# Kernel optimization log

Hardware: AMD Instinct MI355X
Metric: run time of the kernel (lower is better)

Reference implementation:

```python
import jax, jax.numpy as jnp
import numpy as np

B, S, E, H = 2, 2048, 1024, 16
DH = E // H
SCALE = DH ** -0.5

def setup_inputs() -> dict:
    key = jax.random.key(0)
    ks = jax.random.split(key, 5)
    w_std = (2.0 / (E + E)) ** 0.5  # xavier-ish scale
    return {
        'x': jax.random.normal(ks[0], (B, S, E), jnp.float32),
        'Wq': jax.random.normal(ks[1], (E, E), jnp.float32) * w_std,
        'bq': jnp.zeros((E,), jnp.float32),
        'Wk': jax.random.normal(ks[2], (E, E), jnp.float32) * w_std,
        'bk': jnp.zeros((E,), jnp.float32),
        'Wv': jax.random.normal(ks[3], (E, E), jnp.float32) * w_std,
        'bv': jnp.zeros((E,), jnp.float32),
        'Wo': jax.random.normal(ks[4], (E, E), jnp.float32) * w_std,
        'bo': jnp.zeros((E,), jnp.float32),
    }

def reference(x, Wq, bq, Wk, bk, Wv, bv, Wo, bo):
    # self-attention: query = key = value = x; torch Linear: y = x @ W.T + b
    q = (x @ Wq.T + bq) * SCALE            # [B,S,E]
    k = x @ Wk.T + bk
    v = x @ Wv.T + bv
    # split heads -> [B,S,H,DH]
    q = q.reshape(B, S, H, DH)
    k = k.reshape(B, S, H, DH)
    v = v.reshape(B, S, H, DH)
    # explicit attention matrix [B,H,S,S] (faithful to unfused bmm path)
    scores = jnp.einsum('bqhd,bkhd->bhqk', q, k)
    probs = jax.nn.softmax(scores, axis=-1)
    attn = jnp.einsum('bhqk,bkhd->bqhd', probs, v).reshape(B, S, E)
    return attn @ Wo.T + bo                # [B,S,E]
```

## Files before the change

### kernel.cpp

```cpp
#include <hip/hip_runtime.h>
#include <stdint.h>

#define BB 2
#define SS 2048
#define EE 1024
#define HH 16
#define DHD 64
#define MM (BB*SS)
#define QSCALE (0.125f * 1.4426950408889634f)

typedef __bf16 bf16;
typedef __bf16 bf16x8 __attribute__((ext_vector_type(8)));
typedef __bf16 bf16x4 __attribute__((ext_vector_type(4)));
typedef float  f32x4  __attribute__((ext_vector_type(4)));
typedef unsigned short ushort8 __attribute__((ext_vector_type(8)));

#define MFMA16(a,b,c) __builtin_amdgcn_mfma_f32_16x16x32_bf16(a,b,c,0,0,0)

__device__ __forceinline__ void gload_lds16(const void* g, void* l) {
  __builtin_amdgcn_global_load_lds(
      (const __attribute__((address_space(1))) unsigned int*)g,
      (__attribute__((address_space(3))) unsigned int*)l, 16, 0, 0);
}

__device__ __forceinline__ unsigned short f2bf(float f) {
  union { float f; unsigned u; } v; v.f = f;
  return (unsigned short)((v.u + 0x7FFFu + ((v.u >> 16) & 1u)) >> 16);
}

__global__ void convert_kernel(const float* __restrict__ x,
                               const float* __restrict__ wq, const float* __restrict__ wk,
                               const float* __restrict__ wv, const float* __restrict__ wo,
                               unsigned short* __restrict__ xbf,
                               unsigned short* __restrict__ wqb, unsigned short* __restrict__ wkb,
                               unsigned short* __restrict__ wvb, unsigned short* __restrict__ wob) {
  long t = (long)blockIdx.x * blockDim.x + threadIdx.x;
  long base = t * 8;
  const float* src; unsigned short* dst; long off;
  if (base < 4194304L) { src = x; dst = xbf; off = base; }
  else {
    long r = base - 4194304L; int j = (int)(r >> 20); off = r & 1048575L;
    src = (j==0)?wq:(j==1)?wk:(j==2)?wv:wo;
    dst = (j==0)?wqb:(j==1)?wkb:(j==2)?wvb:wob;
  }
  const float4* s4 = (const float4*)(src + off);
  float4 a = s4[0], b = s4[1];
  ushort8 o;
  o[0]=f2bf(a.x); o[1]=f2bf(a.y); o[2]=f2bf(a.z); o[3]=f2bf(a.w);
  o[4]=f2bf(b.x); o[5]=f2bf(b.y); o[6]=f2bf(b.z); o[7]=f2bf(b.w);
  *(ushort8*)(dst + off) = o;
}

#define GS_STAGE(kbuf, kt) { \
    const size_t kb_ = (size_t)(kt) * 64; \
    char* d_ = lds + (kbuf) * 16384 + tid * 16; \
    gload_lds16(a0 + kb_, d_); \
    gload_lds16(a1 + kb_, d_ + 4096); \
    gload_lds16(b0 + kb_, d_ + 8192); \
    gload_lds16(b1 + kb_, d_ + 12288); \
  }

template<bool SWAP>
__device__ __forceinline__ void gemm_kloop(
    const char* a0, const char* a1, const char* b0, const char* b1,
    char* lds, const int tid, const int (&aoff)[4], const int (&boff)[4],
    f32x4 (&acc)[4][4]) {
  GS_STAGE(0, 0);
  for (int kt = 0; kt < 32; ++kt) {
    const int cur = kt & 1;
    if (kt < 31) {
      GS_STAGE(cur ^ 1, kt + 1);
      asm volatile("s_waitcnt vmcnt(4)" ::: "memory");
    } else {
      asm volatile("s_waitcnt vmcnt(0)" ::: "memory");
    }
    __builtin_amdgcn_s_barrier();
    const char* Ts = lds + cur * 16384;
    bf16x8 af[4], bfv[4];
#pragma unroll
    for (int mt=0; mt<4; ++mt) af[mt] = *(const bf16x8*)(Ts + aoff[mt]);
#pragma unroll
    for (int nt=0; nt<4; ++nt) bfv[nt] = *(const bf16x8*)(Ts + boff[nt]);
#pragma unroll
    for (int mt=0; mt<4; ++mt)
#pragma unroll
      for (int nt=0; nt<4; ++nt)
        acc[mt][nt] = SWAP ? MFMA16(bfv[nt], af[mt], acc[mt][nt])
                           : MFMA16(af[mt], bfv[nt], acc[mt][nt]);
    asm volatile("s_waitcnt lgkmcnt(0)" ::: "memory");
    __builtin_amdgcn_s_barrier();
  }
}

__global__ __launch_bounds__(256) void qkv_gemm(
    const bf16* __restrict__ xbf,
    const bf16* __restrict__ wqb, const bf16* __restrict__ wkb, const bf16* __restrict__ wvb,
    const float* __restrict__ bq, const float* __restrict__ bk, const float* __restrict__ bv,
    bf16* __restrict__ Q, bf16* __restrict__ K, bf16* __restrict__ VT) {
  __shared__ char lds[32768] __attribute__((aligned(16)));
  const int tid = threadIdx.x;
  const int bm = blockIdx.y * 128;
  const int bnG = blockIdx.x * 128;
  const int proj = bnG >> 10;
  const int bn = bnG & 1023;
  const bf16* wsel = (proj==0)?wqb:(proj==1)?wkb:wvb;
  const float* bias = (proj==0)?bq:(proj==1)?bk:bv;

  const int lane = tid & 63, w = tid >> 6;
  const int wm = (w>>1)*64, wn = (w&1)*64;
  const int c = lane & 15, g = lane >> 4;

  const int sr = tid >> 2;
  const int scb = ((tid & 3) * 16) ^ ((sr & 3) << 4);
  const char* a0 = (const char*)xbf  + ((size_t)(bm + sr     ) * 1024) * 2 + scb;
  const char* a1 = (const char*)xbf  + ((size_t)(bm + 64 + sr) * 1024) * 2 + scb;
  const char* b0 = (const char*)wsel + ((size_t)(bn + sr     ) * 1024) * 2 + scb;
  const char* b1 = (const char*)wsel + ((size_t)(bn + 64 + sr) * 1024) * 2 + scb;

  int aoff[4], boff[4];
#pragma unroll
  for (int mt=0; mt<4; ++mt) { int rr = wm + mt*16 + c; aoff[mt] = rr*64 + ((g*16) ^ ((rr&3)<<4)); }
#pragma unroll
  for (int nt=0; nt<4; ++nt) { int rr = wn + nt*16 + c; boff[nt] = 8192 + rr*64 + ((g*16) ^ ((rr&3)<<4)); }

  f32x4 acc[4][4];
#pragma unroll
  for (int mt=0; mt<4; ++mt)
#pragma unroll
    for (int nt=0; nt<4; ++nt) acc[mt][nt] = (f32x4){0.f,0.f,0.f,0.f};

  const int bidx = bm >> 11;
  const int srow = bm & 2047;

  if (proj != 2) {
    gemm_kloop<true>(a0, a1, b0, b1, lds, tid, aoff, boff, acc);
    bf16* dst = (proj == 0) ? Q : K;
    const float qs = (proj == 0) ? QSCALE : 1.0f;
#pragma unroll
    for (int nt=0; nt<4; ++nt) {
      const int n0 = bn + wn + nt*16 + g*4;
      const float4 b4 = *(const float4*)(bias + n0);
      const int h = n0 >> 6, d0 = n0 & 63;
#pragma unroll
      for (int mt=0; mt<4; ++mt) {
        const int s = srow + wm + mt*16 + c;
        bf16x4 pk;
        pk[0] = (bf16)((acc[mt][nt][0] + b4.x) * qs);
        pk[1] = (bf16)((acc[mt][nt][1] + b4.y) * qs);
        pk[2] = (bf16)((acc[mt][nt][2] + b4.z) * qs);
        pk[3] = (bf16)((acc[mt][nt][3] + b4.w) * qs);
        *(bf16x4*)(dst + (((size_t)(bidx*16 + h))*2048 + s)*64 + d0) = pk;
      }
    }
  } else {
    gemm_kloop<false>(a0, a1, b0, b1, lds, tid, aoff, boff, acc);
#pragma unroll
    for (int nt=0; nt<4; ++nt) {
      const int n = bn + wn + nt*16 + c;
      const float bv_ = bias[n];
      const int h = n >> 6, d = n & 63;
#pragma unroll
      for (int mt=0; mt<4; ++mt) {
        const int m0 = wm + mt*16 + g*4;
        bf16x4 pk;
#pragma unroll
        for (int r=0;r<4;++r) pk[r] = (bf16)(acc[mt][nt][r] + bv_);
        *(bf16x4*)(VT + (((size_t)(bidx*16 + h))*64 + d)*2048 + (srow + m0)) = pk;
      }
    }
  }
}

__global__ __launch_bounds__(256) void attn_kernel(
    const bf16* __restrict__ Q, const bf16* __restrict__ K,
    const bf16* __restrict__ VT, bf16* __restrict__ attn_out) {
  __shared__ char alds[32768] __attribute__((aligned(16)));
  const int tid = threadIdx.x;
  const int lane = tid & 63, w = tid >> 6;
  const int c = lane & 15, g = lane >> 4;
  const int x7 = c & 7;
  const int bh = blockIdx.y;
  const int qb = blockIdx.x * 64 + w * 16;
  const bf16* Qh = Q + (size_t)bh * 2048 * 64;
  const char* Khb = (const char*)(K  + (size_t)bh * 2048 * 64);
  const char* Vhb = (const char*)(VT + (size_t)bh * 64 * 2048);

  const int srow = tid >> 3, schunk = tid & 7;
  const int ssw = ((schunk ^ (srow & 7)) << 4);
  const char* srcK = Khb + (size_t)srow * 128  + ssw;
  const char* srcV = Vhb + (size_t)srow * 4096 + ssw;

#define ATT_STAGE(buf, kv) { \
    const char* sk_ = srcK + (size_t)(kv) * 128; \
    const char* sv_ = srcV + (size_t)(kv) * 2; \
    char* d_ = alds + (buf) * 16384 + tid * 16; \
    gload_lds16(sk_,            d_); \
    gload_lds16(sk_ + 32*128,   d_ + 4096); \
    gload_lds16(sv_,            d_ + 8192); \
    gload_lds16(sv_ + 32*4096,  d_ + 12288); \
  }

  bf16x8 qf0 = *(const bf16x8*)(Qh + (size_t)(qb + c)*64 + g*8);
  bf16x8 qf1 = *(const bf16x8*)(Qh + (size_t)(qb + c)*64 + 32 + g*8);

  f32x4 o[4];
#pragma unroll
  for (int dt=0; dt<4; ++dt) o[dt] = (f32x4){0.f,0.f,0.f,0.f};
  float m = -1e30f, l = 0.f;

  ATT_STAGE(0, 0);
  for (int t = 0; t < 32; ++t) {
    const int cur = t & 1;
    if (t < 31) {
      ATT_STAGE(cur ^ 1, (t + 1) * 64);
      asm volatile("s_waitcnt vmcnt(4)" ::: "memory");
    } else {
      asm volatile("s_waitcnt vmcnt(0)" ::: "memory");
    }
    __builtin_amdgcn_s_barrier();

    const char* Kl = alds + cur * 16384;
    const char* Vl = Kl + 8192;

    f32x4 st[4];
#pragma unroll
    for (int ks = 0; ks < 4; ++ks) {
      const char* kr = Kl + (ks*16 + c) * 128;
      bf16x8 k0 = *(const bf16x8*)(kr + (((g    ) ^ x7) << 4));
      bf16x8 k1 = *(const bf16x8*)(kr + (((g + 4) ^ x7) << 4));
      f32x4 z = (f32x4){0.f,0.f,0.f,0.f};
      z = MFMA16(k0, qf0, z);
      z = MFMA16(k1, qf1, z);
      st[ks] = z;
    }

    float tmax = -1e30f;
#pragma unroll
    for (int ks = 0; ks < 4; ++ks)
      tmax = fmaxf(tmax, fmaxf(fmaxf(st[ks][0], st[ks][1]), fmaxf(st[ks][2], st[ks][3])));
    tmax = fmaxf(tmax, __shfl_xor(tmax, 16, 64));
    tmax = fmaxf(tmax, __shfl_xor(tmax, 32, 64));
    const float mnew = fmaxf(m, tmax);
    const float corr = __builtin_exp2f(m - mnew);
    float p[4][4]; float ps = 0.f;
#pragma unroll
    for (int ks = 0; ks < 4; ++ks)
#pragma unroll
      for (int r = 0; r < 4; ++r) { p[ks][r] = __builtin_exp2f(st[ks][r] - mnew); ps += p[ks][r]; }
    ps += __shfl_xor(ps, 16, 64);
    ps += __shfl_xor(ps, 32, 64);
    l = l * corr + ps;
    m = mnew;
#pragma unroll
    for (int dt=0; dt<4; ++dt) o[dt] *= corr;

    bf16x8 pfA, pfB;
#pragma unroll
    for (int r = 0; r < 4; ++r) {
      pfA[r] = (bf16)p[0][r]; pfA[4+r] = (bf16)p[1][r];
      pfB[r] = (bf16)p[2][r]; pfB[4+r] = (bf16)p[3][r];
    }

#pragma unroll
    for (int dt = 0; dt < 4; ++dt) {
      const char* vr = Vl + (dt*16 + c) * 128;
      const int i8 = (g & 1) * 8, gh = g >> 1;
      bf16x4 va0 = *(const bf16x4*)(vr + (((gh    ) ^ x7) << 4) + i8);
      bf16x4 va1 = *(const bf16x4*)(vr + (((gh + 2) ^ x7) << 4) + i8);
      bf16x4 vb0 = *(const bf16x4*)(vr + (((gh + 4) ^ x7) << 4) + i8);
      bf16x4 vb1 = *(const bf16x4*)(vr + (((gh + 6) ^ x7) << 4) + i8);
      bf16x8 vfA = __builtin_shufflevector(va0, va1, 0,1,2,3,4,5,6,7);
      bf16x8 vfB = __builtin_shufflevector(vb0, vb1, 0,1,2,3,4,5,6,7);
      o[dt] = MFMA16(vfA, pfA, o[dt]);
      o[dt] = MFMA16(vfB, pfB, o[dt]);
    }

    asm volatile("s_waitcnt lgkmcnt(0)" ::: "memory");
    __builtin_amdgcn_s_barrier();
  }
#undef ATT_STAGE

  const float inv = 1.0f / l;
  const int srow_q = qb + c;
  const int b = bh >> 4, h = bh & 15;
  bf16* outrow = attn_out + ((size_t)(b*2048 + srow_q))*1024 + h*64;
#pragma unroll
  for (int dt=0; dt<4; ++dt) {
    bf16x4 ov;
#pragma unroll
    for (int r=0;r<4;++r) ov[r] = (bf16)(o[dt][r] * inv);
    *(bf16x4*)(outrow + dt*16 + g*4) = ov;
  }
}

__global__ __launch_bounds__(256) void out_gemm(
    const bf16* __restrict__ A, const bf16* __restrict__ W,
    const float* __restrict__ bias, float* __restrict__ out) {
  __shared__ char lds[32768] __attribute__((aligned(16)));
  const int tid = threadIdx.x;
  const int bm = blockIdx.y * 128, bn = blockIdx.x * 128;
  const int lane = tid & 63, w = tid >> 6;
  const int wm = (w>>1)*64, wn = (w&1)*64;
  const int c = lane & 15, g = lane >> 4;

  const int sr = tid >> 2;
  const int scb = ((tid & 3) * 16) ^ ((sr & 3) << 4);
  const char* a0 = (const char*)A + ((size_t)(bm + sr     ) * 1024) * 2 + scb;
  const char* a1 = (const char*)A + ((size_t)(bm + 64 + sr) * 1024) * 2 + scb;
  const char* b0 = (const char*)W + ((size_t)(bn + sr     ) * 1024) * 2 + scb;
  const char* b1 = (const char*)W + ((size_t)(bn + 64 + sr) * 1024) * 2 + scb;

  int aoff[4], boff[4];
#pragma unroll
  for (int mt=0; mt<4; ++mt) { int rr = wm + mt*16 + c; aoff[mt] = rr*64 + ((g*16) ^ ((rr&3)<<4)); }
#pragma unroll
  for (int nt=0; nt<4; ++nt) { int rr = wn + nt*16 + c; boff[nt] = 8192 + rr*64 + ((g*16) ^ ((rr&3)<<4)); }

  f32x4 acc[4][4];
#pragma unroll
  for (int mt=0; mt<4; ++mt)
#pragma unroll
    for (int nt=0; nt<4; ++nt) acc[mt][nt] = (f32x4){0.f,0.f,0.f,0.f};

  gemm_kloop<true>(a0, a1, b0, b1, lds, tid, aoff, boff, acc);

#pragma unroll
  for (int nt=0; nt<4; ++nt) {
    const int n0 = bn + wn + nt*16 + g*4;
    const float4 b4 = *(const float4*)(bias + n0);
#pragma unroll
    for (int mt=0; mt<4; ++mt) {
      const int m0 = bm + wm + mt*16 + c;
      float4 ov;
      ov.x = acc[mt][nt][0] + b4.x;
      ov.y = acc[mt][nt][1] + b4.y;
      ov.z = acc[mt][nt][2] + b4.z;
      ov.w = acc[mt][nt][3] + b4.w;
      *(float4*)(out + (size_t)m0*1024 + n0) = ov;
    }
  }
}

extern "C" void kernel_launch(void* const* d_in, const int* in_sizes, int n_in,
                              void* d_out, int out_size, void* d_ws, size_t ws_size,
                              hipStream_t stream) {
  const float* x  = (const float*)d_in[0];
  const float* Wq = (const float*)d_in[1];
  const float* bq = (const float*)d_in[2];
  const float* Wk = (const float*)d_in[3];
  const float* bk = (const float*)d_in[4];
  const float* Wv = (const float*)d_in[5];
  const float* bv = (const float*)d_in[6];
  const float* Wo = (const float*)d_in[7];
  const float* bo = (const float*)d_in[8];

  char* ws = (char*)d_ws;
  const size_t MiB = 1u << 20;
  unsigned short* xbf = (unsigned short*)(ws);
  unsigned short* wqb = (unsigned short*)(ws +  8*MiB);
  unsigned short* wkb = (unsigned short*)(ws + 10*MiB);
  unsigned short* wvb = (unsigned short*)(ws + 12*MiB);
  unsigned short* wob = (unsigned short*)(ws + 14*MiB);
  bf16* Qb    = (bf16*)(ws + 16*MiB);
  bf16* Kb    = (bf16*)(ws + 24*MiB);
  bf16* VTb   = (bf16*)(ws + 32*MiB);
  bf16* attnb = (bf16*)(ws + 40*MiB);

  convert_kernel<<<4096, 256, 0, stream>>>(x, Wq, Wk, Wv, Wo, xbf, wqb, wkb, wvb, wob);
  qkv_gemm<<<dim3(24, 32), 256, 0, stream>>>(
      (const bf16*)xbf, (const bf16*)wqb, (const bf16*)wkb, (const bf16*)wvb,
      bq, bk, bv, Qb, Kb, VTb);
  attn_kernel<<<dim3(32, 32), 256, 0, stream>>>(Qb, Kb, VTb, attnb);
  out_gemm<<<dim3(8, 32), 256, 0, stream>>>(attnb, (const bf16*)wob, bo, (float*)d_out);
}
```

Measured before the change: 233.0 us.

## Triple-buffer GEMM k-loops and halve out_gemm M-tile for more blocks

The shared GEMM k-loop moves from double to triple buffering in LDS, prefetching two k-tiles ahead and loosening the vmcnt waits, so global loads overlap more with the MFMA work. qkv_gemm LDS grows to 48KB to hold the third buffer. out_gemm gets its own loop with a 64x128 tile instead of 128x128, also triple-buffered, doubling the grid from 256 to 512 blocks to fill more CUs. The costs are more LDS per block, which can limit occupancy, and less reuse per loaded tile in out_gemm.

```diff
diff --git a/kernel.cpp b/kernel.cpp
--- a/kernel.cpp
+++ b/kernel.cpp
@@ -66,10 +66,14 @@
     char* lds, const int tid, const int (&aoff)[4], const int (&boff)[4],
     f32x4 (&acc)[4][4]) {
   GS_STAGE(0, 0);
+  GS_STAGE(1, 1);
+  int cur = 0;
   for (int kt = 0; kt < 32; ++kt) {
-    const int cur = kt & 1;
-    if (kt < 31) {
-      GS_STAGE(cur ^ 1, kt + 1);
+    if (kt < 30) {
+      int sb = cur - 1; if (sb < 0) sb = 2;
+      GS_STAGE(sb, kt + 2);
+      asm volatile("s_waitcnt vmcnt(8)" ::: "memory");
+    } else if (kt == 30) {
       asm volatile("s_waitcnt vmcnt(4)" ::: "memory");
     } else {
       asm volatile("s_waitcnt vmcnt(0)" ::: "memory");
@@ -89,6 +93,7 @@
                            : MFMA16(af[mt], bfv[nt], acc[mt][nt]);
     asm volatile("s_waitcnt lgkmcnt(0)" ::: "memory");
     __builtin_amdgcn_s_barrier();
+    cur = (cur == 2) ? 0 : cur + 1;
   }
 }
 
@@ -97,7 +102,7 @@
     const bf16* __restrict__ wqb, const bf16* __restrict__ wkb, const bf16* __restrict__ wvb,
     const float* __restrict__ bq, const float* __restrict__ bk, const float* __restrict__ bv,
     bf16* __restrict__ Q, bf16* __restrict__ K, bf16* __restrict__ VT) {
-  __shared__ char lds[32768] __attribute__((aligned(16)));
+  __shared__ char lds[49152] __attribute__((aligned(16)));
   const int tid = threadIdx.x;
   const int bm = blockIdx.y * 128;
   const int bnG = blockIdx.x * 128;
@@ -296,41 +301,76 @@
 __global__ __launch_bounds__(256) void out_gemm(
     const bf16* __restrict__ A, const bf16* __restrict__ W,
     const float* __restrict__ bias, float* __restrict__ out) {
-  __shared__ char lds[32768] __attribute__((aligned(16)));
+  __shared__ char lds[36864] __attribute__((aligned(16)));
   const int tid = threadIdx.x;
-  const int bm = blockIdx.y * 128, bn = blockIdx.x * 128;
+  const int bm = blockIdx.y * 64, bn = blockIdx.x * 128;
   const int lane = tid & 63, w = tid >> 6;
-  const int wm = (w>>1)*64, wn = (w&1)*64;
   const int c = lane & 15, g = lane >> 4;
 
   const int sr = tid >> 2;
   const int scb = ((tid & 3) * 16) ^ ((sr & 3) << 4);
   const char* a0 = (const char*)A + ((size_t)(bm + sr     ) * 1024) * 2 + scb;
-  const char* a1 = (const char*)A + ((size_t)(bm + 64 + sr) * 1024) * 2 + scb;
   const char* b0 = (const char*)W + ((size_t)(bn + sr     ) * 1024) * 2 + scb;
   const char* b1 = (const char*)W + ((size_t)(bn + 64 + sr) * 1024) * 2 + scb;
 
-  int aoff[4], boff[4];
-#pragma unroll
-  for (int mt=0; mt<4; ++mt) { int rr = wm + mt*16 + c; aoff[mt] = rr*64 + ((g*16) ^ ((rr&3)<<4)); }
-#pragma unroll
-  for (int nt=0; nt<4; ++nt) { int rr = wn + nt*16 + c; boff[nt] = 8192 + rr*64 + ((g*16) ^ ((rr&3)<<4)); }
-
-  f32x4 acc[4][4];
+#define OUT_STAGE(kbuf, kt) { \
+    const size_t kb_ = (size_t)(kt) * 64; \
+    char* d_ = lds + (kbuf) * 12288 + tid * 16; \
+    gload_lds16(a0 + kb_, d_); \
+    gload_lds16(b0 + kb_, d_ + 4096); \
+    gload_lds16(b1 + kb_, d_ + 8192); \
+  }
+
+  int aoff[4], boff[2];
+#pragma unroll
+  for (int mt=0; mt<4; ++mt) { int rr = mt*16 + c; aoff[mt] = rr*64 + ((g*16) ^ ((rr&3)<<4)); }
+#pragma unroll
+  for (int nt=0; nt<2; ++nt) { int rr = w*32 + nt*16 + c; boff[nt] = 4096 + rr*64 + ((g*16) ^ ((rr&3)<<4)); }
+
+  f32x4 acc[4][2];
 #pragma unroll
   for (int mt=0; mt<4; ++mt)
 #pragma unroll
-    for (int nt=0; nt<4; ++nt) acc[mt][nt] = (f32x4){0.f,0.f,0.f,0.f};
-
-  gemm_kloop<true>(a0, a1, b0, b1, lds, tid, aoff, boff, acc);
-
-#pragma unroll
-  for (int nt=0; nt<4; ++nt) {
-    const int n0 = bn + wn + nt*16 + g*4;
+    for (int nt=0; nt<2; ++nt) acc[mt][nt] = (f32x4){0.f,0.f,0.f,0.f};
+
+  OUT_STAGE(0, 0);
+  OUT_STAGE(1, 1);
+  int cur = 0;
+  for (int kt = 0; kt < 32; ++kt) {
+    if (kt < 30) {
+      int sb = cur - 1; if (sb < 0) sb = 2;
+      OUT_STAGE(sb, kt + 2);
+      asm volatile("s_waitcnt vmcnt(6)" ::: "memory");
+    } else if (kt == 30) {
+      asm volatile("s_waitcnt vmcnt(3)" ::: "memory");
+    } else {
+      asm volatile("s_waitcnt vmcnt(0)" ::: "memory");
+    }
+    __builtin_amdgcn_s_barrier();
+    const char* Ts = lds + cur * 12288;
+    bf16x8 af[4], bfv[2];
+#pragma unroll
+    for (int mt=0; mt<4; ++mt) af[mt] = *(const bf16x8*)(Ts + aoff[mt]);
+#pragma unroll
+    for (int nt=0; nt<2; ++nt) bfv[nt] = *(const bf16x8*)(Ts + boff[nt]);
+#pragma unroll
+    for (int mt=0; mt<4; ++mt)
+#pragma unroll
+      for (int nt=0; nt<2; ++nt)
+        acc[mt][nt] = MFMA16(bfv[nt], af[mt], acc[mt][nt]);
+    asm volatile("s_waitcnt lgkmcnt(0)" ::: "memory");
+    __builtin_amdgcn_s_barrier();
+    cur = (cur == 2) ? 0 : cur + 1;
+  }
+#undef OUT_STAGE
+
+#pragma unroll
+  for (int nt=0; nt<2; ++nt) {
+    const int n0 = bn + w*32 + nt*16 + g*4;
     const float4 b4 = *(const float4*)(bias + n0);
 #pragma unroll
     for (int mt=0; mt<4; ++mt) {
-      const int m0 = bm + wm + mt*16 + c;
+      const int m0 = bm + mt*16 + c;
       float4 ov;
       ov.x = acc[mt][nt][0] + b4.x;
       ov.y = acc[mt][nt][1] + b4.y;
@@ -371,5 +411,5 @@
       (const bf16*)xbf, (const bf16*)wqb, (const bf16*)wkb, (const bf16*)wvb,
       bq, bk, bv, Qb, Kb, VTb);
   attn_kernel<<<dim3(32, 32), 256, 0, stream>>>(Qb, Kb, VTb, attnb);
-  out_gemm<<<dim3(8, 32), 256, 0, stream>>>(attnb, (const bf16*)wob, bo, (float*)d_out);
-}
+  out_gemm<<<dim3(8, 64), 256, 0, stream>>>(attnb, (const bf16*)wob, bo, (float*)d_out);
+}
```

Measured after the change: 227.7 us. -2.3%, faster.
